# Performance work log

Measured on AMD Instinct MI355X. Metric: run time of the kernel, lower is better.

## Reference

```python
import jax, jax.numpy as jnp
import numpy as np

N_HEAD = 16
N_EMBD = 1024
HEAD_DIM = N_EMBD // N_HEAD


def setup_inputs() -> dict:
    key = jax.random.key(0)
    k1, k2, k3 = jax.random.split(key, 3)
    B, T, C = 2, 2048, N_EMBD
    x = jax.random.normal(k1, (B, T, C), dtype=jnp.float32)
    # Linear weights stored as (in, out); torch nn.Linear weight is (out,in), y = x @ W.T.
    # We store the already-transposed form so reference does x @ w.
    w_attn = jax.random.normal(k2, (C, 3 * C), dtype=jnp.float32) * (1.0 / np.sqrt(C))
    w_proj = jax.random.normal(k3, (C, C), dtype=jnp.float32) * (1.0 / np.sqrt(C))
    return {"x": x, "w_attn": w_attn, "w_proj": w_proj}


def reference(x, w_attn, w_proj):
    B, T, C = x.shape
    qkv = x @ w_attn                          # [B,T,3C]
    q, k, v = jnp.split(qkv, 3, axis=2)
    # [B,T,C] -> [B,H,T,D]
    def heads(t):
        return t.reshape(B, T, N_HEAD, HEAD_DIM).transpose(0, 2, 1, 3)
    q, k, v = heads(q), heads(k), heads(v)
    scale = 1.0 / np.sqrt(HEAD_DIM)
    att = jnp.einsum('bhqd,bhkd->bhqk', q, k) * scale  # [B,H,T,T]
    causal = jnp.tril(jnp.ones((T, T), dtype=bool))
    att = jnp.where(causal, att, -jnp.inf)
    att = jax.nn.softmax(att, axis=-1)
    y = jnp.einsum('bhqk,bhkd->bhqd', att, v)          # [B,H,T,D]
    y = y.transpose(0, 2, 1, 3).reshape(B, T, C)
    return y @ w_proj
```

## Files before the change

kernel.cpp:

```cpp
#include <hip/hip_runtime.h>
#include <hip/hip_bf16.h>
#include <stdint.h>

typedef unsigned short u16;
typedef unsigned int u32;
typedef unsigned long long u64;
typedef float f32x4 __attribute__((ext_vector_type(4)));
typedef float f32x16 __attribute__((ext_vector_type(16)));
typedef short bf16x8 __attribute__((ext_vector_type(8)));
typedef u32 u32x4 __attribute__((ext_vector_type(4)));

#define MFMA(a, b, c) __builtin_amdgcn_mfma_f32_16x16x32_bf16((a), (b), (c), 0, 0, 0)
#define MFMA32(a, b, c) __builtin_amdgcn_mfma_f32_32x32x16_bf16((a), (b), (c), 0, 0, 0)

__device__ __forceinline__ void gll16(const void* g, void* lds) {
  __builtin_amdgcn_global_load_lds(
      (const __attribute__((address_space(1))) u32*)(uintptr_t)g,
      (__attribute__((address_space(3))) u32*)(uintptr_t)lds, 16, 0, 0);
}

__device__ __forceinline__ u16 f2b(float f) {
  union { __hip_bfloat16 h; u16 u; } cv;
  cv.h = __float2bfloat16(f);
  return cv.u;
}
__device__ __forceinline__ float b2f(u16 b) {
  union { u32 u; float f; } cv;
  cv.u = (u32)b << 16;
  return cv.f;
}
__device__ __forceinline__ u32 cvtpk(float lo, float hi) {
  u32 r;
  asm("v_cvt_pk_bf16_f32 %0, %1, %2" : "=v"(r) : "v"(lo), "v"(hi));
  return r;
}

__device__ __forceinline__ int sw(int r) { return ((r ^ (r >> 3)) & 7) << 4; }

__global__ __launch_bounds__(256) void k_cvt(const float* __restrict__ in,
                                             u16* __restrict__ out, int n4) {
  int i = blockIdx.x * 256 + threadIdx.x;
  if (i >= n4) return;
  const float4 v = reinterpret_cast<const float4*>(in)[i];
  u32 lo = (u32)f2b(v.x) | ((u32)f2b(v.y) << 16);
  u32 hi = (u32)f2b(v.z) | ((u32)f2b(v.w) << 16);
  reinterpret_cast<uint2*>(out)[i] = make_uint2(lo, hi);
}

__global__ __launch_bounds__(256) void k_trcvt(const float* __restrict__ in,
                                               u16* __restrict__ out, int R, int C) {
  __shared__ float tile[64][65];
  const int tid = threadIdx.x;
  const int r0 = blockIdx.y * 64, c0 = blockIdx.x * 64;
  const int tr = tid >> 4;
  const int tc4 = (tid & 15) * 4;
#pragma unroll
  for (int i = 0; i < 4; ++i) {
    const float4 v = *reinterpret_cast<const float4*>(
        &in[(size_t)(r0 + i * 16 + tr) * C + c0 + tc4]);
    tile[i * 16 + tr][tc4 + 0] = v.x;
    tile[i * 16 + tr][tc4 + 1] = v.y;
    tile[i * 16 + tr][tc4 + 2] = v.z;
    tile[i * 16 + tr][tc4 + 3] = v.w;
  }
  __syncthreads();
#pragma unroll
  for (int i = 0; i < 4; ++i) {
    const int c = i * 16 + tr;
    const int r4 = tc4;
    u32 lo = (u32)f2b(tile[r4 + 0][c]) | ((u32)f2b(tile[r4 + 1][c]) << 16);
    u32 hi = (u32)f2b(tile[r4 + 2][c]) | ((u32)f2b(tile[r4 + 3][c]) << 16);
    *reinterpret_cast<uint2*>(&out[(size_t)(c0 + c) * R + r0 + r4]) =
        make_uint2(lo, hi);
  }
}

__global__ __launch_bounds__(512, 1) void k_gemm1(const u16* __restrict__ A,
                                                  const u16* __restrict__ Bt,
                                                  u16* __restrict__ C) {
  __shared__ u16 As[2][256 * 64];
  __shared__ u16 Bs[2][192 * 64];
  const int tid = threadIdx.x;
  const int lane = tid & 63;
  const int w = tid >> 6;
  const int wm = w >> 2, wn = w & 3;
  const int l15 = lane & 15, lg = lane >> 4;

  const int bid = blockIdx.x;
  const int lin = (bid & 7) * 32 + (bid >> 3);
  const int bm = lin >> 4, bn = lin & 15;
  const size_t brow = (size_t)bm * 256, bcol = (size_t)bn * 192;

  const int sr = tid >> 3;
  const int scb = (tid & 7) * 16;
  const int gcol = (scb ^ sw(sr)) >> 1;
  const u16* Ag[4];
#pragma unroll
  for (int i = 0; i < 4; ++i) Ag[i] = A + (brow + i * 64 + sr) * 1024 + gcol;
  const u16* Bg[3];
#pragma unroll
  for (int i = 0; i < 3; ++i) Bg[i] = Bt + (bcol + i * 64 + sr) * 1024 + gcol;

  f32x4 acc[8][3] = {};

#pragma unroll
  for (int i = 0; i < 4; ++i) gll16(Ag[i], (char*)As[0] + i * 8192 + tid * 16);
#pragma unroll
  for (int i = 0; i < 3; ++i) gll16(Bg[i], (char*)Bs[0] + i * 8192 + tid * 16);
  asm volatile("s_waitcnt vmcnt(0) lgkmcnt(0)" ::: "memory");
  __builtin_amdgcn_s_barrier();
  __builtin_amdgcn_sched_barrier(0);

  for (int kt = 0; kt < 16; ++kt) {
    const int cur = kt & 1;
    const char* as = (const char*)As[cur];
    const char* bs = (const char*)Bs[cur];
    char* asn = (char*)As[cur ^ 1];
    char* bsn = (char*)Bs[cur ^ 1];
    const bool more = (kt + 1 < 16);
    const int ko = (kt + 1) * 64;

    bf16x8 bfr[3][2];
#pragma unroll
    for (int n = 0; n < 3; ++n) {
      const int row = wn * 48 + n * 16 + l15;
#pragma unroll
      for (int kh = 0; kh < 2; ++kh)
        bfr[n][kh] = *(const bf16x8*)(bs + row * 128 +
                                      ((kh * 64 + lg * 16) ^ sw(row)));
    }
#define GPHASE(MB, STAGE_A, STAGE_B, LAST)                                    \
    {                                                                         \
      bf16x8 af[2][2];                                                        \
      _Pragma("unroll")                                                       \
      for (int mm = 0; mm < 2; ++mm) {                                        \
        const int row = wm * 128 + (MB + mm) * 16 + l15;                      \
        _Pragma("unroll")                                                     \
        for (int kh = 0; kh < 2; ++kh)                                        \
          af[mm][kh] = *(const bf16x8*)(as + row * 128 +                      \
                                        ((kh * 64 + lg * 16) ^ sw(row)));     \
      }                                                                       \
      if (STAGE_A && more) {                                                  \
        _Pragma("unroll")                                                     \
        for (int i = 0; i < 4; ++i)                                           \
          gll16(Ag[i] + ko, asn + i * 8192 + tid * 16);                       \
      }                                                                       \
      if (STAGE_B && more) {                                                  \
        _Pragma("unroll")                                                     \
        for (int i = 0; i < 3; ++i)                                           \
          gll16(Bg[i] + ko, bsn + i * 8192 + tid * 16);                       \
      }                                                                       \
      __builtin_amdgcn_s_setprio(1);                                          \
      _Pragma("unroll")                                                       \
      for (int mm = 0; mm < 2; ++mm)                                          \
        _Pragma("unroll")                                                     \
        for (int n = 0; n < 3; ++n) {                                         \
          acc[MB + mm][n] = MFMA(af[mm][0], bfr[n][0], acc[MB + mm][n]);      \
          acc[MB + mm][n] = MFMA(af[mm][1], bfr[n][1], acc[MB + mm][n]);      \
        }                                                                     \
      __builtin_amdgcn_s_setprio(0);                                          \
      if (LAST) {                                                             \
        asm volatile("s_waitcnt vmcnt(0) lgkmcnt(0)" ::: "memory");           \
      }                                                                       \
      __builtin_amdgcn_s_barrier();                                           \
    }
    GPHASE(0, 1, 0, 0)
    GPHASE(2, 0, 1, 0)
    GPHASE(4, 0, 0, 0)
    GPHASE(6, 0, 0, 1)
#undef GPHASE
    __builtin_amdgcn_sched_barrier(0);
  }

#pragma unroll
  for (int m = 0; m < 8; ++m) {
    const size_t row = brow + wm * 128 + m * 16 + lg * 4;
#pragma unroll
    for (int n = 0; n < 3; ++n) {
      const size_t col = bcol + wn * 48 + n * 16 + l15;
#pragma unroll
      for (int r = 0; r < 4; ++r)
        C[(row + r) * 3072 + col] = f2b(acc[m][n][r]);
    }
  }
}

__global__ __launch_bounds__(256) void k_gemm2(const u16* __restrict__ A,
                                               const u16* __restrict__ Bt,
                                               float* __restrict__ C) {
  __shared__ u16 As[2][128 * 64];
  __shared__ u16 Bs[2][128 * 64];
  const int tid = threadIdx.x;
  const int lane = tid & 63;
  const int w = tid >> 6;
  const int wm = w >> 1, wn = w & 1;
  const int l15 = lane & 15, lg = lane >> 4;

  const int bid = blockIdx.x;
  const int lin = (bid & 7) * 32 + (bid >> 3);
  const int bm = lin >> 3, bn = lin & 7;
  const size_t brow = (size_t)bm * 128, bcol = (size_t)bn * 128;

  const int sr = tid >> 3;
  const int scb = (tid & 7) * 16;
  const u16* Ag[4];
  const u16* Bg[4];
#pragma unroll
  for (int i = 0; i < 4; ++i) {
    const int row = i * 32 + sr;
    const int gcol = (scb ^ sw(row)) >> 1;
    Ag[i] = A + (brow + row) * 1024 + gcol;
    Bg[i] = Bt + (bcol + row) * 1024 + gcol;
  }

  f32x4 acc[4][4] = {};

#pragma unroll
  for (int i = 0; i < 4; ++i) gll16(Ag[i], (char*)As[0] + i * 4096 + tid * 16);
#pragma unroll
  for (int i = 0; i < 4; ++i) gll16(Bg[i], (char*)Bs[0] + i * 4096 + tid * 16);
  asm volatile("s_waitcnt vmcnt(0) lgkmcnt(0)" ::: "memory");
  __builtin_amdgcn_s_barrier();
  __builtin_amdgcn_sched_barrier(0);

  for (int kt = 0; kt < 16; ++kt) {
    const int cur = kt & 1;
    const char* as = (const char*)As[cur];
    const char* bs = (const char*)Bs[cur];
    char* asn = (char*)As[cur ^ 1];
    char* bsn = (char*)Bs[cur ^ 1];
    const bool more = (kt + 1 < 16);
    const int ko = (kt + 1) * 64;

    bf16x8 bfr[4][2];
#pragma unroll
    for (int n = 0; n < 4; ++n) {
      const int row = wn * 64 + n * 16 + l15;
#pragma unroll
      for (int kh = 0; kh < 2; ++kh)
        bfr[n][kh] = *(const bf16x8*)(bs + row * 128 +
                                      ((kh * 64 + lg * 16) ^ sw(row)));
    }
#define G2PHASE(MB, STAGE_A, STAGE_B, LAST)                                   \
    {                                                                         \
      bf16x8 af[2];                                                           \
      {                                                                       \
        const int row = wm * 64 + (MB) * 16 + l15;                            \
        _Pragma("unroll")                                                     \
        for (int kh = 0; kh < 2; ++kh)                                        \
          af[kh] = *(const bf16x8*)(as + row * 128 +                          \
                                    ((kh * 64 + lg * 16) ^ sw(row)));         \
      }                                                                       \
      if (STAGE_A && more) {                                                  \
        _Pragma("unroll")                                                     \
        for (int i = 0; i < 4; ++i)                                           \
          gll16(Ag[i] + ko, asn + i * 4096 + tid * 16);                       \
      }                                                                       \
      if (STAGE_B && more) {                                                  \
        _Pragma("unroll")                                                     \
        for (int i = 0; i < 4; ++i)                                           \
          gll16(Bg[i] + ko, bsn + i * 4096 + tid * 16);                       \
      }                                                                       \
      __builtin_amdgcn_s_setprio(1);                                          \
      _Pragma("unroll")                                                       \
      for (int n = 0; n < 4; ++n) {                                           \
        acc[MB][n] = MFMA(af[0], bfr[n][0], acc[MB][n]);                      \
        acc[MB][n] = MFMA(af[1], bfr[n][1], acc[MB][n]);                      \
      }                                                                       \
      __builtin_amdgcn_s_setprio(0);                                          \
      if (LAST) {                                                             \
        asm volatile("s_waitcnt vmcnt(0) lgkmcnt(0)" ::: "memory");           \
      }                                                                       \
      __builtin_amdgcn_s_barrier();                                           \
    }
    G2PHASE(0, 1, 0, 0)
    G2PHASE(1, 0, 1, 0)
    G2PHASE(2, 0, 0, 0)
    G2PHASE(3, 0, 0, 1)
#undef G2PHASE
    __builtin_amdgcn_sched_barrier(0);
  }

#pragma unroll
  for (int m = 0; m < 4; ++m) {
    const size_t row = brow + wm * 64 + m * 16 + lg * 4;
#pragma unroll
    for (int n = 0; n < 4; ++n) {
      const size_t col = bcol + wn * 64 + n * 16 + l15;
#pragma unroll
      for (int r = 0; r < 4; ++r)
        C[(row + r) * 1024 + col] = acc[m][n][r];
    }
  }
}

__global__ __launch_bounds__(512, 1) void k_attn(const u16* __restrict__ qkv,
                                                 u16* __restrict__ y) {
  __shared__ u16 Kl[3][64 * 64];
  __shared__ u16 Vt[2][64 * 64];
  __shared__ float Om[4][64][33];
  __shared__ float Lm[4][2][32];
  const int tid = threadIdx.x;
  const int lane = tid & 63;
  const int w = tid >> 6;
  const int qsub = w & 3, tsub = w >> 2;
  const int l31 = lane & 31, hi = lane >> 5;

  const int lin = blockIdx.x;
  const int xcd = lin & 7;
  const int idx = lin >> 3;
  const int bh = xcd * 4 + (idx >> 3);
  const int pidx = idx & 7;
  const int b = bh >> 4, h = bh & 15;

  const u16* Qg = qkv + (size_t)(b * 2048) * 3072 + h * 64;
  const u16* Kg = Qg + 1024;
  const u16* Vg = Qg + 2048;

  const int srow = tid >> 3;
  const int scol = (((tid & 7) * 16) ^ sw(srow)) >> 1;
  const bool vstage = (tid < 256);
  const int t2 = (tid & 255) >> 3;
  const int d8 = (tid & 7) * 8;

  bf16x8 vone;
#pragma unroll
  for (int j = 0; j < 8; ++j) vone[j] = (short)0x3F80;

  const int trow = tsub * 32 + l31;
  int koff[4];
#pragma unroll
  for (int ks = 0; ks < 4; ++ks)
    koff[ks] = trow * 128 + (((ks * 16 + hi * 8) * 2) ^ sw(trow));
  int voff[2][2];
#pragma unroll
  for (int db = 0; db < 2; ++db) {
    const int dl = db * 32 + l31;
#pragma unroll
    for (int ks = 0; ks < 2; ++ks)
      voff[db][ks] = dl * 128 + (((tsub * 32 + ks * 16 + hi * 8) * 2) ^ sw(dl));
  }

  for (int pass = 0; pass < 2; ++pass) {
    const int qi = pass ? (15 - pidx) : pidx;
    const int nt = 2 * (qi + 1);
    const int qb = qi * 128;
    const int qrow = qb + qsub * 32 + l31;

    bf16x8 aq[4];
#pragma unroll
    for (int ks = 0; ks < 4; ++ks) {
      bf16x8 v = *(const bf16x8*)&Qg[(size_t)qrow * 3072 + ks * 16 + hi * 8];
#pragma unroll
      for (int j = 0; j < 8; ++j)
        v[j] = (short)f2b(b2f((u16)v[j]) * 0.18033688011112042f);
      aq[ks] = v;
    }

    f32x16 acc0 = {}, acc1 = {}, accl = {};

    bf16x8 va0, va1;
    {
      bf16x8 v00, v01;
      if (vstage) {
        v00 = *(const bf16x8*)&Vg[(size_t)(2 * t2) * 3072 + d8];
        v01 = *(const bf16x8*)&Vg[(size_t)(2 * t2 + 1) * 3072 + d8];
        va0 = *(const bf16x8*)&Vg[(size_t)(64 + 2 * t2) * 3072 + d8];
        va1 = *(const bf16x8*)&Vg[(size_t)(64 + 2 * t2 + 1) * 3072 + d8];
      }
      gll16(Kg + (size_t)srow * 3072 + scol, (u16*)Kl[0] + tid * 8);
      gll16(Kg + (size_t)(64 + srow) * 3072 + scol, (u16*)Kl[1] + tid * 8);
      if (vstage) {
#pragma unroll
        for (int j = 0; j < 8; ++j) {
          const int d = d8 + j;
          const u32 val = (u32)(u16)v00[j] | ((u32)(u16)v01[j] << 16);
          *(u32*)((char*)Vt[0] + ((d * 128 + t2 * 4) ^ sw(d))) = val;
        }
      }
    }
    asm volatile("s_waitcnt vmcnt(1) lgkmcnt(0)" ::: "memory");
    __builtin_amdgcn_s_barrier();
    __builtin_amdgcn_sched_barrier(0);

    const char* kR = (const char*)Kl[0];
    const char* kN = (const char*)Kl[1];
    char* kN2 = (char*)Kl[2];
    const char* vR = (const char*)Vt[0];
    char* vW = (char*)Vt[1];

    for (int t = 0; t < nt; ++t) {
      const int tf = (t + 2 < 31 ? t + 2 : 31);
      bf16x8 vf0, vf1;
      if (vstage) {
        vf0 = *(const bf16x8*)&Vg[(size_t)(tf * 64 + 2 * t2) * 3072 + d8];
        vf1 = *(const bf16x8*)&Vg[(size_t)(tf * 64 + 2 * t2 + 1) * 3072 + d8];
      }
      gll16(Kg + (size_t)(tf * 64 + srow) * 3072 + scol, (u16*)kN2 + tid * 8);

      f32x16 s = {};
#pragma unroll
      for (int ks = 0; ks < 4; ++ks) {
        const bf16x8 kf = *(const bf16x8*)(kR + koff[ks]);
        s = MFMA32(kf, aq[ks], s);
      }

      float p[16];
      if (t >= nt - 2) {
#pragma unroll
        for (int r = 0; r < 16; ++r) {
          const int kkg = t * 64 + tsub * 32 + (r & 3) + 8 * (r >> 2) + 4 * hi;
          p[r] = exp2f(kkg > qrow ? -1e30f : s[r]);
        }
      } else {
#pragma unroll
        for (int r = 0; r < 16; ++r) p[r] = exp2f(s[r]);
      }

      const u32 X0 = cvtpk(p[0], p[1]),   X1 = cvtpk(p[2], p[3]);
      const u32 X2 = cvtpk(p[4], p[5]),   X3 = cvtpk(p[6], p[7]);
      const u32 X4 = cvtpk(p[8], p[9]),   X5 = cvtpk(p[10], p[11]);
      const u32 X6 = cvtpk(p[12], p[13]), X7 = cvtpk(p[14], p[15]);
      const u32 sx0 = (u32)__shfl_xor((int)X0, 32);
      const u32 sx1 = (u32)__shfl_xor((int)X1, 32);
      const u32 sx2 = (u32)__shfl_xor((int)X2, 32);
      const u32 sx3 = (u32)__shfl_xor((int)X3, 32);
      const u32 sx4 = (u32)__shfl_xor((int)X4, 32);
      const u32 sx5 = (u32)__shfl_xor((int)X5, 32);
      const u32 sx6 = (u32)__shfl_xor((int)X6, 32);
      const u32 sx7 = (u32)__shfl_xor((int)X7, 32);
      union { u32x4 u; bf16x8 h; } c0, c1;
      c0.u[0] = hi ? sx2 : X0;
      c0.u[1] = hi ? sx3 : X1;
      c0.u[2] = hi ? X2 : sx0;
      c0.u[3] = hi ? X3 : sx1;
      c1.u[0] = hi ? sx6 : X4;
      c1.u[1] = hi ? sx7 : X5;
      c1.u[2] = hi ? X6 : sx4;
      c1.u[3] = hi ? X7 : sx5;
      const bf16x8 pb0 = c0.h, pb1 = c1.h;

      accl = MFMA32(vone, pb0, accl);
      accl = MFMA32(vone, pb1, accl);
      const bf16x8 vb00 = *(const bf16x8*)(vR + voff[0][0]);
      const bf16x8 vb01 = *(const bf16x8*)(vR + voff[0][1]);
      const bf16x8 vb10 = *(const bf16x8*)(vR + voff[1][0]);
      const bf16x8 vb11 = *(const bf16x8*)(vR + voff[1][1]);
      acc0 = MFMA32(vb00, pb0, acc0);
      acc0 = MFMA32(vb01, pb1, acc0);
      acc1 = MFMA32(vb10, pb0, acc1);
      acc1 = MFMA32(vb11, pb1, acc1);

      if (vstage && t < nt - 1) {
#pragma unroll
        for (int j = 0; j < 8; ++j) {
          const int d = d8 + j;
          const u32 val = (u32)(u16)va0[j] | ((u32)(u16)va1[j] << 16);
          *(u32*)(vW + ((d * 128 + t2 * 4) ^ sw(d))) = val;
        }
      }
      va0 = vf0; va1 = vf1;
      const char* kt = kR; kR = kN; kN = kN2; kN2 = (char*)kt;
      char* vt_ = (char*)vR; vR = vW; vW = vt_;

      asm volatile("s_waitcnt vmcnt(1) lgkmcnt(0)" ::: "memory");
      __builtin_amdgcn_s_barrier();
      __builtin_amdgcn_sched_barrier(0);
    }

    asm volatile("s_waitcnt vmcnt(0) lgkmcnt(0)" ::: "memory");
    __builtin_amdgcn_s_barrier();
    __builtin_amdgcn_sched_barrier(0);

    if (tsub == 1) {
#pragma unroll
      for (int r = 0; r < 16; ++r) {
        const int d = (r & 3) + 8 * (r >> 2) + 4 * hi;
        Om[qsub][d][l31] = acc0[r];
        Om[qsub][32 + d][l31] = acc1[r];
      }
      Lm[qsub][1][l31] = accl[0];
    } else {
      Lm[qsub][0][l31] = accl[0];
    }
    __syncthreads();
    if (tsub == 0) {
      const float linv = 1.0f / (Lm[qsub][0][l31] + Lm[qsub][1][l31]);
#pragma unroll
      for (int r = 0; r < 16; ++r) {
        const int d = (r & 3) + 8 * (r >> 2) + 4 * hi;
        Om[qsub][d][l31] = (acc0[r] + Om[qsub][d][l31]) * linv;
        Om[qsub][32 + d][l31] = (acc1[r] + Om[qsub][32 + d][l31]) * linv;
      }
    }
    __syncthreads();
    {
      const int qloc = tid >> 2;
      const int dgr = (tid & 3) * 16;
      const size_t yo = (size_t)(b * 2048 + qb + qloc) * 1024 + h * 64 + dgr;
      u32 o[8];
#pragma unroll
      for (int jj = 0; jj < 8; ++jj)
        o[jj] = cvtpk(Om[qloc >> 5][dgr + 2 * jj][qloc & 31],
                      Om[qloc >> 5][dgr + 2 * jj + 1][qloc & 31]);
      u32x4 s0 = {o[0], o[1], o[2], o[3]};
      u32x4 s1 = {o[4], o[5], o[6], o[7]};
      *(u32x4*)&y[yo] = s0;
      *(u32x4*)&y[yo + 8] = s1;
    }
    __syncthreads();
  }
}

extern "C" void kernel_launch(void* const* d_in, const int* in_sizes, int n_in,
                              void* d_out, int out_size, void* d_ws, size_t ws_size,
                              hipStream_t stream) {
  const float* x  = (const float*)d_in[0];
  const float* wa = (const float*)d_in[1];
  const float* wp = (const float*)d_in[2];
  float* out = (float*)d_out;

  u16* xb  = (u16*)d_ws;
  u16* wat = xb + (size_t)4096 * 1024;
  u16* wpt = wat + (size_t)3072 * 1024;
  u16* qkv = wpt + (size_t)1024 * 1024;
  u16* yb  = qkv + (size_t)4096 * 3072;

  k_cvt<<<4096, 256, 0, stream>>>(x, xb, 4096 * 1024 / 4);
  k_trcvt<<<dim3(3072 / 64, 1024 / 64), 256, 0, stream>>>(wa, wat, 1024, 3072);
  k_trcvt<<<dim3(1024 / 64, 1024 / 64), 256, 0, stream>>>(wp, wpt, 1024, 1024);

  k_gemm1<<<256, 512, 0, stream>>>(xb, wat, qkv);

  k_attn<<<256, 512, 0, stream>>>(qkv, yb);

  k_gemm2<<<256, 256, 0, stream>>>(yb, wpt, out);
}
```

Baseline: 107.6 us.

## Restructure QKV GEMM into 256x256 tiles with quadrant-staged LDS pipeline

The QKV projection GEMM moves from 256x192 tiles on 256 blocks to 256x256 tiles on 192 blocks. Each k-step is split into four quadrant phases, and each phase issues a half-tile global-to-LDS stage for a later k-step, using partial vmcnt waits instead of full drains. The goals are more operand reuse per block and better overlap of loads with MFMA work. In exchange, 192 blocks no longer cover all 256 CUs, and the wait and barrier accounting becomes intricate and fragile.

After: 118.1 us. 1.1x slower.

```diff
diff --git a/kernel.cpp b/kernel.cpp
--- a/kernel.cpp
+++ b/kernel.cpp
@@ -79,110 +79,118 @@
                                                   const u16* __restrict__ Bt,
                                                   u16* __restrict__ C) {
   __shared__ u16 As[2][256 * 64];
-  __shared__ u16 Bs[2][192 * 64];
+  __shared__ u16 Bs[2][256 * 64];
   const int tid = threadIdx.x;
   const int lane = tid & 63;
   const int w = tid >> 6;
-  const int wm = w >> 2, wn = w & 3;
+  const int wm = w >> 2;
+  const int wn = w & 3;
   const int l15 = lane & 15, lg = lane >> 4;
 
   const int bid = blockIdx.x;
-  const int lin = (bid & 7) * 32 + (bid >> 3);
-  const int bm = lin >> 4, bn = lin & 15;
-  const size_t brow = (size_t)bm * 256, bcol = (size_t)bn * 192;
+  const int lin = (bid & 7) * 24 + (bid >> 3);
+  const int bm = lin / 12, bn = lin % 12;
+  const size_t brow = (size_t)bm * 256, bcol = (size_t)bn * 256;
 
   const int sr = tid >> 3;
   const int scb = (tid & 7) * 16;
   const int gcol = (scb ^ sw(sr)) >> 1;
-  const u16* Ag[4];
-#pragma unroll
-  for (int i = 0; i < 4; ++i) Ag[i] = A + (brow + i * 64 + sr) * 1024 + gcol;
-  const u16* Bg[3];
-#pragma unroll
-  for (int i = 0; i < 3; ++i) Bg[i] = Bt + (bcol + i * 64 + sr) * 1024 + gcol;
-
-  f32x4 acc[8][3] = {};
-
-#pragma unroll
-  for (int i = 0; i < 4; ++i) gll16(Ag[i], (char*)As[0] + i * 8192 + tid * 16);
-#pragma unroll
-  for (int i = 0; i < 3; ++i) gll16(Bg[i], (char*)Bs[0] + i * 8192 + tid * 16);
-  asm volatile("s_waitcnt vmcnt(0) lgkmcnt(0)" ::: "memory");
+  const u16* baseA = A + (brow + sr) * 1024 + gcol;
+  const u16* baseB = Bt + (bcol + sr) * 1024 + gcol;
+
+  f32x4 acc[2][4][2][2] = {};
+
+#define STG_A(KT, H, CB)                                                      \
+  {                                                                           \
+    _Pragma("unroll")                                                         \
+    for (int p = 0; p < 2; ++p)                                               \
+      gll16(baseA + (size_t)((H) * 128 + p * 64) * 1024 + (KT) * 64,          \
+            (u16*)As + (CB) * 16384 + ((H) * 128 + p * 64) * 64 + tid * 8);   \
+  }
+#define STG_B(KT, H, CB)                                                      \
+  {                                                                           \
+    _Pragma("unroll")                                                         \
+    for (int p = 0; p < 2; ++p)                                               \
+      gll16(baseB + (size_t)((H) * 128 + p * 64) * 1024 + (KT) * 64,          \
+            (u16*)Bs + (CB) * 16384 + ((H) * 128 + p * 64) * 64 + tid * 8);   \
+  }
+
+#define QPH(CB, MH, NH, DO_STG, DO_VM)                                        \
+  {                                                                           \
+    bf16x8 af[4][2];                                                          \
+    _Pragma("unroll")                                                         \
+    for (int mq = 0; mq < 4; ++mq) {                                          \
+      const int row = (MH) * 128 + wm * 64 + mq * 16 + l15;                   \
+      _Pragma("unroll")                                                       \
+      for (int kh = 0; kh < 2; ++kh)                                          \
+        af[mq][kh] = *(const bf16x8*)((const char*)As + (CB) * 32768 +        \
+                         row * 128 + ((kh * 64 + lg * 16) ^ sw(row)));        \
+    }                                                                         \
+    bf16x8 bv[2][2];                                                          \
+    _Pragma("unroll")                                                         \
+    for (int nq = 0; nq < 2; ++nq) {                                          \
+      const int row = (NH) * 128 + wn * 32 + nq * 16 + l15;                   \
+      _Pragma("unroll")                                                       \
+      for (int kh = 0; kh < 2; ++kh)                                          \
+        bv[nq][kh] = *(const bf16x8*)((const char*)Bs + (CB) * 32768 +        \
+                         row * 128 + ((kh * 64 + lg * 16) ^ sw(row)));        \
+    }                                                                         \
+    DO_STG;                                                                   \
+    __builtin_amdgcn_s_setprio(1);                                            \
+    _Pragma("unroll")                                                         \
+    for (int mq = 0; mq < 4; ++mq)                                            \
+      _Pragma("unroll")                                                       \
+      for (int nq = 0; nq < 2; ++nq) {                                        \
+        acc[MH][mq][NH][nq] = MFMA(af[mq][0], bv[nq][0], acc[MH][mq][NH][nq]);\
+        acc[MH][mq][NH][nq] = MFMA(af[mq][1], bv[nq][1], acc[MH][mq][NH][nq]);\
+      }                                                                       \
+    __builtin_amdgcn_s_setprio(0);                                            \
+    if (DO_VM) { asm volatile("s_waitcnt vmcnt(4)" ::: "memory"); }           \
+    __builtin_amdgcn_s_barrier();                                             \
+    __builtin_amdgcn_sched_barrier(0);                                        \
+  }
+
+  STG_A(0, 0, 0)
+  STG_B(0, 0, 0)
+  STG_B(0, 1, 0)
+  STG_A(0, 1, 0)
+  asm volatile("s_waitcnt vmcnt(4)" ::: "memory");
   __builtin_amdgcn_s_barrier();
   __builtin_amdgcn_sched_barrier(0);
 
-  for (int kt = 0; kt < 16; ++kt) {
-    const int cur = kt & 1;
-    const char* as = (const char*)As[cur];
-    const char* bs = (const char*)Bs[cur];
-    char* asn = (char*)As[cur ^ 1];
-    char* bsn = (char*)Bs[cur ^ 1];
-    const bool more = (kt + 1 < 16);
-    const int ko = (kt + 1) * 64;
-
-    bf16x8 bfr[3][2];
-#pragma unroll
-    for (int n = 0; n < 3; ++n) {
-      const int row = wn * 48 + n * 16 + l15;
-#pragma unroll
-      for (int kh = 0; kh < 2; ++kh)
-        bfr[n][kh] = *(const bf16x8*)(bs + row * 128 +
-                                      ((kh * 64 + lg * 16) ^ sw(row)));
-    }
-#define GPHASE(MB, STAGE_A, STAGE_B, LAST)                                    \
-    {                                                                         \
-      bf16x8 af[2][2];                                                        \
-      _Pragma("unroll")                                                       \
-      for (int mm = 0; mm < 2; ++mm) {                                        \
-        const int row = wm * 128 + (MB + mm) * 16 + l15;                      \
-        _Pragma("unroll")                                                     \
-        for (int kh = 0; kh < 2; ++kh)                                        \
-          af[mm][kh] = *(const bf16x8*)(as + row * 128 +                      \
-                                        ((kh * 64 + lg * 16) ^ sw(row)));     \
-      }                                                                       \
-      if (STAGE_A && more) {                                                  \
-        _Pragma("unroll")                                                     \
-        for (int i = 0; i < 4; ++i)                                           \
-          gll16(Ag[i] + ko, asn + i * 8192 + tid * 16);                       \
-      }                                                                       \
-      if (STAGE_B && more) {                                                  \
-        _Pragma("unroll")                                                     \
-        for (int i = 0; i < 3; ++i)                                           \
-          gll16(Bg[i] + ko, bsn + i * 8192 + tid * 16);                       \
-      }                                                                       \
-      __builtin_amdgcn_s_setprio(1);                                          \
-      _Pragma("unroll")                                                       \
-      for (int mm = 0; mm < 2; ++mm)                                          \
-        _Pragma("unroll")                                                     \
-        for (int n = 0; n < 3; ++n) {                                         \
-          acc[MB + mm][n] = MFMA(af[mm][0], bfr[n][0], acc[MB + mm][n]);      \
-          acc[MB + mm][n] = MFMA(af[mm][1], bfr[n][1], acc[MB + mm][n]);      \
-        }                                                                     \
-      __builtin_amdgcn_s_setprio(0);                                          \
-      if (LAST) {                                                             \
-        asm volatile("s_waitcnt vmcnt(0) lgkmcnt(0)" ::: "memory");           \
-      }                                                                       \
-      __builtin_amdgcn_s_barrier();                                           \
-    }
-    GPHASE(0, 1, 0, 0)
-    GPHASE(2, 0, 1, 0)
-    GPHASE(4, 0, 0, 0)
-    GPHASE(6, 0, 0, 1)
-#undef GPHASE
-    __builtin_amdgcn_sched_barrier(0);
-  }
-
-#pragma unroll
-  for (int m = 0; m < 8; ++m) {
-    const size_t row = brow + wm * 128 + m * 16 + lg * 4;
-#pragma unroll
-    for (int n = 0; n < 3; ++n) {
-      const size_t col = bcol + wn * 48 + n * 16 + l15;
-#pragma unroll
-      for (int r = 0; r < 4; ++r)
-        C[(row + r) * 3072 + col] = f2b(acc[m][n][r]);
-    }
-  }
+  for (int i = 0; i < 8; ++i) {
+    const int kto = 2 * i + 1;
+    const int ktn = (2 * i + 2 < 16) ? 2 * i + 2 : 15;
+    QPH(0, 0, 0, STG_A(kto, 0, 1), 1)
+    QPH(0, 0, 1, STG_B(kto, 0, 1), 1)
+    QPH(0, 1, 0, STG_B(kto, 1, 1), 0)
+    QPH(0, 1, 1, STG_A(kto, 1, 1), 1)
+    QPH(1, 0, 0, STG_A(ktn, 0, 0), 1)
+    QPH(1, 0, 1, STG_B(ktn, 0, 0), 1)
+    QPH(1, 1, 0, STG_B(ktn, 1, 0), 0)
+    QPH(1, 1, 1, STG_A(ktn, 1, 0), 1)
+  }
+#undef QPH
+#undef STG_A
+#undef STG_B
+
+  asm volatile("s_waitcnt vmcnt(0)" ::: "memory");
+
+#pragma unroll
+  for (int mh = 0; mh < 2; ++mh)
+#pragma unroll
+    for (int mq = 0; mq < 4; ++mq) {
+      const size_t row = brow + mh * 128 + wm * 64 + mq * 16 + lg * 4;
+#pragma unroll
+      for (int nh = 0; nh < 2; ++nh)
+#pragma unroll
+        for (int nq = 0; nq < 2; ++nq) {
+          const size_t col = bcol + nh * 128 + wn * 32 + nq * 16 + l15;
+#pragma unroll
+          for (int r = 0; r < 4; ++r)
+            C[(row + r) * 3072 + col] = f2b(acc[mh][mq][nh][nq][r]);
+        }
+    }
 }
 
 __global__ __launch_bounds__(256) void k_gemm2(const u16* __restrict__ A,
@@ -530,7 +538,7 @@
   k_trcvt<<<dim3(3072 / 64, 1024 / 64), 256, 0, stream>>>(wa, wat, 1024, 3072);
   k_trcvt<<<dim3(1024 / 64, 1024 / 64), 256, 0, stream>>>(wp, wpt, 1024, 1024);
 
-  k_gemm1<<<256, 512, 0, stream>>>(xb, wat, qkv);
+  k_gemm1<<<192, 512, 0, stream>>>(xb, wat, qkv);
 
   k_attn<<<256, 512, 0, stream>>>(qkv, yb);
 
```

## Replace QKV GEMM with templated 128x128-tile kernel shared with output projection

Applied to the files above, without the earlier changes.

Drops the dedicated 256x192-tile, 512-thread QKV projection kernel. Both GEMMs now use one templated 128x128-tile, 256-thread kernel whose column count and output type (bf16 or f32) are template parameters. The QKV GEMM launches 768 smaller blocks instead of 256 large ones, giving more blocks per CU and better load balance. The cost is lower per-block data reuse and more global and LDS traffic per FLOP.

Result: slower. 112.1 us (+4.2%).

```diff
diff --git a/kernel.cpp b/kernel.cpp
--- a/kernel.cpp
+++ b/kernel.cpp
@@ -75,119 +75,12 @@
   }
 }
 
-__global__ __launch_bounds__(512, 1) void k_gemm1(const u16* __restrict__ A,
-                                                  const u16* __restrict__ Bt,
-                                                  u16* __restrict__ C) {
-  __shared__ u16 As[2][256 * 64];
-  __shared__ u16 Bs[2][192 * 64];
-  const int tid = threadIdx.x;
-  const int lane = tid & 63;
-  const int w = tid >> 6;
-  const int wm = w >> 2, wn = w & 3;
-  const int l15 = lane & 15, lg = lane >> 4;
-
-  const int bid = blockIdx.x;
-  const int lin = (bid & 7) * 32 + (bid >> 3);
-  const int bm = lin >> 4, bn = lin & 15;
-  const size_t brow = (size_t)bm * 256, bcol = (size_t)bn * 192;
-
-  const int sr = tid >> 3;
-  const int scb = (tid & 7) * 16;
-  const int gcol = (scb ^ sw(sr)) >> 1;
-  const u16* Ag[4];
-#pragma unroll
-  for (int i = 0; i < 4; ++i) Ag[i] = A + (brow + i * 64 + sr) * 1024 + gcol;
-  const u16* Bg[3];
-#pragma unroll
-  for (int i = 0; i < 3; ++i) Bg[i] = Bt + (bcol + i * 64 + sr) * 1024 + gcol;
-
-  f32x4 acc[8][3] = {};
-
-#pragma unroll
-  for (int i = 0; i < 4; ++i) gll16(Ag[i], (char*)As[0] + i * 8192 + tid * 16);
-#pragma unroll
-  for (int i = 0; i < 3; ++i) gll16(Bg[i], (char*)Bs[0] + i * 8192 + tid * 16);
-  asm volatile("s_waitcnt vmcnt(0) lgkmcnt(0)" ::: "memory");
-  __builtin_amdgcn_s_barrier();
-  __builtin_amdgcn_sched_barrier(0);
-
-  for (int kt = 0; kt < 16; ++kt) {
-    const int cur = kt & 1;
-    const char* as = (const char*)As[cur];
-    const char* bs = (const char*)Bs[cur];
-    char* asn = (char*)As[cur ^ 1];
-    char* bsn = (char*)Bs[cur ^ 1];
-    const bool more = (kt + 1 < 16);
-    const int ko = (kt + 1) * 64;
-
-    bf16x8 bfr[3][2];
-#pragma unroll
-    for (int n = 0; n < 3; ++n) {
-      const int row = wn * 48 + n * 16 + l15;
-#pragma unroll
-      for (int kh = 0; kh < 2; ++kh)
-        bfr[n][kh] = *(const bf16x8*)(bs + row * 128 +
-                                      ((kh * 64 + lg * 16) ^ sw(row)));
-    }
-#define GPHASE(MB, STAGE_A, STAGE_B, LAST)                                    \
-    {                                                                         \
-      bf16x8 af[2][2];                                                        \
-      _Pragma("unroll")                                                       \
-      for (int mm = 0; mm < 2; ++mm) {                                        \
-        const int row = wm * 128 + (MB + mm) * 16 + l15;                      \
-        _Pragma("unroll")                                                     \
-        for (int kh = 0; kh < 2; ++kh)                                        \
-          af[mm][kh] = *(const bf16x8*)(as + row * 128 +                      \
-                                        ((kh * 64 + lg * 16) ^ sw(row)));     \
-      }                                                                       \
-      if (STAGE_A && more) {                                                  \
-        _Pragma("unroll")                                                     \
-        for (int i = 0; i < 4; ++i)                                           \
-          gll16(Ag[i] + ko, asn + i * 8192 + tid * 16);                       \
-      }                                                                       \
-      if (STAGE_B && more) {                                                  \
-        _Pragma("unroll")                                                     \
-        for (int i = 0; i < 3; ++i)                                           \
-          gll16(Bg[i] + ko, bsn + i * 8192 + tid * 16);                       \
-      }                                                                       \
-      __builtin_amdgcn_s_setprio(1);                                          \
-      _Pragma("unroll")                                                       \
-      for (int mm = 0; mm < 2; ++mm)                                          \
-        _Pragma("unroll")                                                     \
-        for (int n = 0; n < 3; ++n) {                                         \
-          acc[MB + mm][n] = MFMA(af[mm][0], bfr[n][0], acc[MB + mm][n]);      \
-          acc[MB + mm][n] = MFMA(af[mm][1], bfr[n][1], acc[MB + mm][n]);      \
-        }                                                                     \
-      __builtin_amdgcn_s_setprio(0);                                          \
-      if (LAST) {                                                             \
-        asm volatile("s_waitcnt vmcnt(0) lgkmcnt(0)" ::: "memory");           \
-      }                                                                       \
-      __builtin_amdgcn_s_barrier();                                           \
-    }
-    GPHASE(0, 1, 0, 0)
-    GPHASE(2, 0, 1, 0)
-    GPHASE(4, 0, 0, 0)
-    GPHASE(6, 0, 0, 1)
-#undef GPHASE
-    __builtin_amdgcn_sched_barrier(0);
-  }
-
-#pragma unroll
-  for (int m = 0; m < 8; ++m) {
-    const size_t row = brow + wm * 128 + m * 16 + lg * 4;
-#pragma unroll
-    for (int n = 0; n < 3; ++n) {
-      const size_t col = bcol + wn * 48 + n * 16 + l15;
-#pragma unroll
-      for (int r = 0; r < 4; ++r)
-        C[(row + r) * 3072 + col] = f2b(acc[m][n][r]);
-    }
-  }
-}
-
-__global__ __launch_bounds__(256) void k_gemm2(const u16* __restrict__ A,
+template <int NCOLS, int F32OUT>
+__global__ __launch_bounds__(256) void k_gemmT(const u16* __restrict__ A,
                                                const u16* __restrict__ Bt,
-                                               float* __restrict__ C) {
+                                               void* __restrict__ Cout) {
+  constexpr int NBN = NCOLS / 128;
+  constexpr int NBLK = 32 * NBN;
   __shared__ u16 As[2][128 * 64];
   __shared__ u16 Bs[2][128 * 64];
   const int tid = threadIdx.x;
@@ -197,8 +90,8 @@
   const int l15 = lane & 15, lg = lane >> 4;
 
   const int bid = blockIdx.x;
-  const int lin = (bid & 7) * 32 + (bid >> 3);
-  const int bm = lin >> 3, bn = lin & 7;
+  const int lin = (bid & 7) * (NBLK / 8) + (bid >> 3);
+  const int bm = lin / NBN, bn = lin % NBN;
   const size_t brow = (size_t)bm * 128, bcol = (size_t)bn * 128;
 
   const int sr = tid >> 3;
@@ -288,8 +181,12 @@
     for (int n = 0; n < 4; ++n) {
       const size_t col = bcol + wn * 64 + n * 16 + l15;
 #pragma unroll
-      for (int r = 0; r < 4; ++r)
-        C[(row + r) * 1024 + col] = acc[m][n][r];
+      for (int r = 0; r < 4; ++r) {
+        if (F32OUT)
+          ((float*)Cout)[(row + r) * NCOLS + col] = acc[m][n][r];
+        else
+          ((u16*)Cout)[(row + r) * NCOLS + col] = f2b(acc[m][n][r]);
+      }
     }
   }
 }
@@ -530,9 +427,9 @@
   k_trcvt<<<dim3(3072 / 64, 1024 / 64), 256, 0, stream>>>(wa, wat, 1024, 3072);
   k_trcvt<<<dim3(1024 / 64, 1024 / 64), 256, 0, stream>>>(wp, wpt, 1024, 1024);
 
-  k_gemm1<<<256, 512, 0, stream>>>(xb, wat, qkv);
+  k_gemmT<3072, 0><<<768, 256, 0, stream>>>(xb, wat, qkv);
 
   k_attn<<<256, 512, 0, stream>>>(qkv, yb);
 
-  k_gemm2<<<256, 256, 0, stream>>>(yb, wpt, out);
-}
+  k_gemmT<1024, 1><<<256, 256, 0, stream>>>(yb, wpt, out);
+}
```

## Split attention into 64-row query tiles with 256-thread blocks, two per CU

Applied to the files above, without the earlier changes.

The attention kernel now handles 64 query rows per pass with 4 waves instead of 128 rows with 8 waves. It launches twice as many blocks and allows two blocks per CU, and aliases the output-reduction buffers onto the K/V staging LDS to fit. This is meant to improve load balance across the causal triangle and let one block's barrier waits overlap with another's work. The cost is that each K/V tile is loaded and reused by fewer query rows, which raises global traffic, and each thread now issues two K loads per tile, so the vmcnt wait counts were retuned.

New measurement: 104.7 us. 1.03x faster.

```diff
diff --git a/kernel.cpp b/kernel.cpp
--- a/kernel.cpp
+++ b/kernel.cpp
@@ -294,33 +294,36 @@
   }
 }
 
-__global__ __launch_bounds__(512, 1) void k_attn(const u16* __restrict__ qkv,
+__global__ __launch_bounds__(256, 2) void k_attn(const u16* __restrict__ qkv,
                                                  u16* __restrict__ y) {
-  __shared__ u16 Kl[3][64 * 64];
-  __shared__ u16 Vt[2][64 * 64];
-  __shared__ float Om[4][64][33];
-  __shared__ float Lm[4][2][32];
+  __shared__ char smem[40960];
+  char* KlB = smem;
+  char* VtB = smem + 24576;
+  float (*Om)[64][33] = (float (*)[64][33])smem;
+  float (*Lm)[2][32] = (float (*)[2][32])(smem + 16896);
+
   const int tid = threadIdx.x;
   const int lane = tid & 63;
   const int w = tid >> 6;
-  const int qsub = w & 3, tsub = w >> 2;
+  const int qsub = w & 1, tsub = w >> 1;
   const int l31 = lane & 31, hi = lane >> 5;
 
-  const int lin = blockIdx.x;
-  const int xcd = lin & 7;
-  const int idx = lin >> 3;
-  const int bh = xcd * 4 + (idx >> 3);
-  const int pidx = idx & 7;
+  const int bid = blockIdx.x;
+  const int xcd = bid & 7;
+  const int idx = bid >> 3;
+  const int bh = xcd * 4 + (idx >> 4);
+  const int pidx = idx & 15;
   const int b = bh >> 4, h = bh & 15;
 
   const u16* Qg = qkv + (size_t)(b * 2048) * 3072 + h * 64;
   const u16* Kg = Qg + 1024;
   const u16* Vg = Qg + 2048;
 
-  const int srow = tid >> 3;
-  const int scol = (((tid & 7) * 16) ^ sw(srow)) >> 1;
-  const bool vstage = (tid < 256);
-  const int t2 = (tid & 255) >> 3;
+  const int slotA = tid, slotB = 256 + tid;
+  const int srA = slotA >> 3, srB = slotB >> 3;
+  const int scA = (((slotA & 7) * 16) ^ sw(srA)) >> 1;
+  const int scB = (((slotB & 7) * 16) ^ sw(srB)) >> 1;
+  const int t2 = tid >> 3;
   const int d8 = (tid & 7) * 8;
 
   bf16x8 vone;
@@ -342,9 +345,9 @@
   }
 
   for (int pass = 0; pass < 2; ++pass) {
-    const int qi = pass ? (15 - pidx) : pidx;
-    const int nt = 2 * (qi + 1);
-    const int qb = qi * 128;
+    const int qi = pass ? (31 - pidx) : pidx;
+    const int nt = qi + 1;
+    const int qb = qi * 64;
     const int qrow = qb + qsub * 32 + l31;
 
     bf16x8 aq[4];
@@ -361,42 +364,38 @@
 
     bf16x8 va0, va1;
     {
-      bf16x8 v00, v01;
-      if (vstage) {
-        v00 = *(const bf16x8*)&Vg[(size_t)(2 * t2) * 3072 + d8];
-        v01 = *(const bf16x8*)&Vg[(size_t)(2 * t2 + 1) * 3072 + d8];
-        va0 = *(const bf16x8*)&Vg[(size_t)(64 + 2 * t2) * 3072 + d8];
-        va1 = *(const bf16x8*)&Vg[(size_t)(64 + 2 * t2 + 1) * 3072 + d8];
+      const int t1c = (1 < qi ? 1 : qi) * 64;
+      bf16x8 v00 = *(const bf16x8*)&Vg[(size_t)(2 * t2) * 3072 + d8];
+      bf16x8 v01 = *(const bf16x8*)&Vg[(size_t)(2 * t2 + 1) * 3072 + d8];
+      va0 = *(const bf16x8*)&Vg[(size_t)(t1c + 2 * t2) * 3072 + d8];
+      va1 = *(const bf16x8*)&Vg[(size_t)(t1c + 2 * t2 + 1) * 3072 + d8];
+      gll16(Kg + (size_t)srA * 3072 + scA, (u16*)KlB + slotA * 8);
+      gll16(Kg + (size_t)srB * 3072 + scB, (u16*)KlB + slotB * 8);
+      gll16(Kg + (size_t)(t1c + srA) * 3072 + scA, (u16*)(KlB + 8192) + slotA * 8);
+      gll16(Kg + (size_t)(t1c + srB) * 3072 + scB, (u16*)(KlB + 8192) + slotB * 8);
+#pragma unroll
+      for (int j = 0; j < 8; ++j) {
+        const int d = d8 + j;
+        const u32 val = (u32)(u16)v00[j] | ((u32)(u16)v01[j] << 16);
+        *(u32*)(VtB + ((d * 128 + t2 * 4) ^ sw(d))) = val;
       }
-      gll16(Kg + (size_t)srow * 3072 + scol, (u16*)Kl[0] + tid * 8);
-      gll16(Kg + (size_t)(64 + srow) * 3072 + scol, (u16*)Kl[1] + tid * 8);
-      if (vstage) {
-#pragma unroll
-        for (int j = 0; j < 8; ++j) {
-          const int d = d8 + j;
-          const u32 val = (u32)(u16)v00[j] | ((u32)(u16)v01[j] << 16);
-          *(u32*)((char*)Vt[0] + ((d * 128 + t2 * 4) ^ sw(d))) = val;
-        }
-      }
-    }
-    asm volatile("s_waitcnt vmcnt(1) lgkmcnt(0)" ::: "memory");
+    }
+    asm volatile("s_waitcnt vmcnt(2) lgkmcnt(0)" ::: "memory");
     __builtin_amdgcn_s_barrier();
     __builtin_amdgcn_sched_barrier(0);
 
-    const char* kR = (const char*)Kl[0];
-    const char* kN = (const char*)Kl[1];
-    char* kN2 = (char*)Kl[2];
-    const char* vR = (const char*)Vt[0];
-    char* vW = (char*)Vt[1];
+    const char* kR = KlB;
+    const char* kN = KlB + 8192;
+    char* kN2 = KlB + 16384;
+    const char* vR = VtB;
+    char* vW = VtB + 8192;
 
     for (int t = 0; t < nt; ++t) {
-      const int tf = (t + 2 < 31 ? t + 2 : 31);
-      bf16x8 vf0, vf1;
-      if (vstage) {
-        vf0 = *(const bf16x8*)&Vg[(size_t)(tf * 64 + 2 * t2) * 3072 + d8];
-        vf1 = *(const bf16x8*)&Vg[(size_t)(tf * 64 + 2 * t2 + 1) * 3072 + d8];
-      }
-      gll16(Kg + (size_t)(tf * 64 + srow) * 3072 + scol, (u16*)kN2 + tid * 8);
+      const int tf = (t + 2 < 31 ? t + 2 : 31) * 64;
+      const bf16x8 vf0 = *(const bf16x8*)&Vg[(size_t)(tf + 2 * t2) * 3072 + d8];
+      const bf16x8 vf1 = *(const bf16x8*)&Vg[(size_t)(tf + 2 * t2 + 1) * 3072 + d8];
+      gll16(Kg + (size_t)(tf + srA) * 3072 + scA, (u16*)kN2 + slotA * 8);
+      gll16(Kg + (size_t)(tf + srB) * 3072 + scB, (u16*)kN2 + slotB * 8);
 
       f32x16 s = {};
 #pragma unroll
@@ -406,7 +405,7 @@
       }
 
       float p[16];
-      if (t >= nt - 2) {
+      if (t == nt - 1) {
 #pragma unroll
         for (int r = 0; r < 16; ++r) {
           const int kkg = t * 64 + tsub * 32 + (r & 3) + 8 * (r >> 2) + 4 * hi;
@@ -451,7 +450,7 @@
       acc1 = MFMA32(vb10, pb0, acc1);
       acc1 = MFMA32(vb11, pb1, acc1);
 
-      if (vstage && t < nt - 1) {
+      if (t < nt - 1) {
 #pragma unroll
         for (int j = 0; j < 8; ++j) {
           const int d = d8 + j;
@@ -460,10 +459,10 @@
         }
       }
       va0 = vf0; va1 = vf1;
-      const char* kt = kR; kR = kN; kN = kN2; kN2 = (char*)kt;
+      const char* kt_ = kR; kR = kN; kN = kN2; kN2 = (char*)kt_;
       char* vt_ = (char*)vR; vR = vW; vW = vt_;
 
-      asm volatile("s_waitcnt vmcnt(1) lgkmcnt(0)" ::: "memory");
+      asm volatile("s_waitcnt vmcnt(4) lgkmcnt(0)" ::: "memory");
       __builtin_amdgcn_s_barrier();
       __builtin_amdgcn_sched_barrier(0);
     }
@@ -532,7 +531,7 @@
 
   k_gemm1<<<256, 512, 0, stream>>>(xb, wat, qkv);
 
-  k_attn<<<256, 512, 0, stream>>>(qkv, yb);
+  k_attn<<<512, 256, 0, stream>>>(qkv, yb);
 
   k_gemm2<<<256, 256, 0, stream>>>(yb, wpt, out);
 }
```
